# Kernel tuning notes

Hardware: AMD Instinct MI355X
Metric: run time of the kernel (lower is better)

## Reference

```python
import jax, jax.numpy as jnp
import numpy as np

K = 20
EPS = 1e-5
SLOPE = 0.2


def get_graph_feature(x, k):
    # x: [B, N, C]. DGCNN: knn on negative squared distance, gather, concat(nbr-ctr, ctr).
    sq = jnp.sum(x * x, axis=-1)                              # [B,N]
    inner = jnp.einsum('bnc,bmc->bnm', x, x)                  # [B,N,N]
    pdist = 2.0 * inner - sq[:, :, None] - sq[:, None, :]     # -||xi-xj||^2
    idx = jax.lax.top_k(pdist, k)[1]                          # [B,N,k] nearest (incl. self)
    b = jnp.arange(x.shape[0])[:, None, None]
    nbr = x[b, idx]                                           # [B,N,k,C]
    ctr = jnp.broadcast_to(x[:, :, None, :], nbr.shape)
    return jnp.concatenate([nbr - ctr, ctr], axis=-1)         # [B,N,k,2C]


def edgeconv(x, W, gamma, beta, mean, var):
    # 1x1 Conv2d (no bias) + BatchNorm2d (eval mode) + LeakyReLU(0.2) + max over k
    feat = get_graph_feature(x, K)                            # [B,N,k,2C]
    y = jnp.einsum('bnkc,oc->bnko', feat, W)                  # [B,N,k,O]
    y = (y - mean) * (gamma / jnp.sqrt(var + EPS)) + beta
    y = jnp.where(y >= 0, y, SLOPE * y)
    return jnp.max(y, axis=2)                                 # [B,N,O]


def dgcnn_pass(x, p1, p2, p3):
    x = edgeconv(x, *p1)
    x = edgeconv(x, *p2)
    x = edgeconv(x, *p3)
    return x                                                  # [B,N,F3]


def attention(emb, W_att):
    # SimGNN attention pooling (batched)
    ctx = jnp.tanh(jnp.mean(jnp.einsum('bnf,fg->bng', emb, W_att), axis=1))  # [B,F]
    s = jax.nn.sigmoid(jnp.einsum('bnf,bf->bn', emb, ctx))                   # [B,N]
    return jnp.einsum('bnf,bn->bf', emb, s)                                  # [B,F]


def tensor_network(e1, e2, W_t, W_block, bias):
    scoring = jnp.einsum('bf,fgt,bg->bt', e1, W_t, e2)        # [B,T]
    comb = jnp.concatenate([e1, e2], axis=1)                  # [B,2F]
    block = jnp.einsum('tf,bf->bt', W_block, comb)            # [B,T]
    return jax.nn.relu(scoring + block + bias)


def setup_inputs() -> dict:
    key = jax.random.key(0)
    ks = jax.random.split(key, 16)
    B, N, C = 8, 2048, 12
    F = 64
    T = 16
    d = {}
    d['graph1'] = jax.random.normal(ks[0], (B, N, C), jnp.float32)
    d['graph2'] = jax.random.normal(ks[1], (B, N, C), jnp.float32)
    d['W1'] = jax.random.normal(ks[2], (F, 2 * C), jnp.float32) * 0.1
    d['g1'] = jax.random.uniform(ks[3], (F,), jnp.float32, 0.5, 1.5)
    d['b1'] = jax.random.normal(ks[4], (F,), jnp.float32) * 0.1
    d['m1'] = jnp.zeros((F,), jnp.float32)
    d['v1'] = jnp.ones((F,), jnp.float32)
    d['W2'] = jax.random.normal(ks[5], (F, 2 * F), jnp.float32) * 0.1
    d['g2'] = jax.random.uniform(ks[6], (F,), jnp.float32, 0.5, 1.5)
    d['b2'] = jax.random.normal(ks[7], (F,), jnp.float32) * 0.1
    d['m2'] = jnp.zeros((F,), jnp.float32)
    d['v2'] = jnp.ones((F,), jnp.float32)
    d['W3'] = jax.random.normal(ks[8], (F, 2 * F), jnp.float32) * 0.1
    d['g3'] = jax.random.uniform(ks[9], (F,), jnp.float32, 0.5, 1.5)
    d['b3'] = jax.random.normal(ks[10], (F,), jnp.float32) * 0.1
    d['m3'] = jnp.zeros((F,), jnp.float32)
    d['v3'] = jnp.ones((F,), jnp.float32)
    d['W_att'] = jax.random.normal(ks[11], (F, F), jnp.float32) * 0.1
    d['W_tensor'] = jax.random.normal(ks[12], (F, F, T), jnp.float32) * 0.05
    d['W_block'] = jax.random.normal(ks[13], (T, 2 * F), jnp.float32) * 0.1
    d['bias_tn'] = jax.random.normal(ks[14], (T,), jnp.float32) * 0.1
    return d


def reference(graph1, graph2, W1, g1, b1, m1, v1, W2, g2, b2, m2, v2,
              W3, g3, b3, m3, v3, W_att, W_tensor, W_block, bias_tn):
    p1 = (W1, g1, b1, m1, v1)
    p2 = (W2, g2, b2, m2, v2)
    p3 = (W3, g3, b3, m3, v3)
    emb1 = dgcnn_pass(graph1, p1, p2, p3)   # [B,N,F]
    emb2 = dgcnn_pass(graph2, p1, p2, p3)
    e1 = attention(emb1, W_att)             # [B,F]
    e2 = attention(emb2, W_att)
    return tensor_network(e1, e2, W_tensor, W_block, bias_tn)  # [B,T]
```

## Files before the change

kernel.cpp:

```cpp
#include <hip/hip_runtime.h>
#include <hip/hip_bf16.h>
#include <float.h>

#define DEV __device__ __forceinline__

using f32x4 = __attribute__((ext_vector_type(4))) float;
using f4v   = __attribute__((ext_vector_type(4))) float;
using bfrag = __attribute__((ext_vector_type(8))) short;
using hfrag = __attribute__((ext_vector_type(8))) _Float16;
using us8   = __attribute__((ext_vector_type(8))) unsigned short;

DEV unsigned short f2bf(float f) {
  unsigned u = __builtin_bit_cast(unsigned, f);
  u += 0x7FFFu + ((u >> 16) & 1u);
  return (unsigned short)(u >> 16);
}
DEV float bf2f(unsigned short h) {
  unsigned u = ((unsigned)h) << 16;
  return __builtin_bit_cast(float, u);
}
DEV f32x4 mfma_bf(bfrag a, bfrag b, f32x4 c) {
  return __builtin_amdgcn_mfma_f32_16x16x32_bf16(a, b, c, 0, 0, 0);
}
DEV f32x4 mfma_h(hfrag a, hfrag b, f32x4 c) {
  return __builtin_amdgcn_mfma_f32_16x16x32_f16(a, b, c, 0, 0, 0);
}
DEV float readlane_f(float v, int l) {
  return __builtin_bit_cast(float,
      __builtin_amdgcn_readlane(__builtin_bit_cast(int, v), l));
}

template<int RB>
DEV unsigned swz(int row, int colb) {
  return (unsigned)(row * RB) +
         (((unsigned)colb) ^ (((unsigned)(row << 4)) & (unsigned)(RB - 1)));
}
template<int RB>
DEV bfrag ldfragB(const unsigned short* base, int row, int kcol) {
  return *(const bfrag*)((const char*)base + swz<RB>(row, kcol * 2));
}
template<int RB>
DEV hfrag ldfragH(const _Float16* base, int row, int kcol) {
  return *(const hfrag*)((const char*)base + swz<RB>(row, kcol * 2));
}

template<int BYTES>
DEV void cpyN(const char* __restrict__ g, char* __restrict__ l, int tid) {
  if constexpr (BYTES >= 8192) {
#pragma unroll
    for (int o = 0; o < BYTES; o += 8192)
      *(us8*)(l + o + tid * 16) = *(const us8*)(g + o + tid * 16);
  } else {
    const int o = tid * 16;
    if (o < BYTES) *(us8*)(l + o) = *(const us8*)(g + o);
  }
}

DEV void bitonic64(float& v, int& ix, int lane) {
#pragma unroll
  for (int k = 2; k <= 64; k <<= 1) {
#pragma unroll
    for (int j = k >> 1; j > 0; j >>= 1) {
      const float ov = __shfl_xor(v, j);
      const int   oi = __shfl_xor(ix, j);
      const bool up = (lane & k) != 0;
      const bool iWin = (v > ov) || (v == ov && ix < oi);
      const bool keepBetter = (((lane & j) == 0) != up);
      if (iWin != keepBetter) { v = ov; ix = oi; }
    }
  }
}

template<int C>
DEV const float* xbase(const float* xA, const float* xB, int b) {
  return (b < 8) ? xA + (size_t)b * 2048 * C
                 : xB + (size_t)(b - 8) * 2048 * C;
}

template<int C>
__global__ __launch_bounds__(256)
void sq_kernel(const float* __restrict__ xA, const float* __restrict__ xB,
               float* __restrict__ sq) {
  const int i = blockIdx.x * 256 + threadIdx.x;
  const int b = i >> 11, n = i & 2047;
  const float* r = xbase<C>(xA, xB, b) + (size_t)n * C;
  float s = 0.f;
#pragma unroll
  for (int c = 0; c < C; c += 4) {
    f4v v = *(const f4v*)(r + c);
    s += v[0] * v[0] + v[1] * v[1] + v[2] * v[2] + v[3] * v[3];
  }
  sq[i] = s;
}

template<int C, int C32>
__global__ __launch_bounds__(256)
void cvt_kernel(const float* __restrict__ xA, const float* __restrict__ xB,
                char* __restrict__ xhl) {
  constexpr int CH8 = C32 / 8, RB = C32 * 2, HB = 64 * RB;
  const int idx = blockIdx.x * 256 + threadIdx.x;
  const int chunk = idx & (CH8 - 1);
  const int rg = idx / CH8;
  const int b = rg >> 11, n = rg & 2047;
  const float* src = xbase<C>(xA, xB, b) + (size_t)n * C;
  const int cb = chunk * 8;
  float f[8];
  if constexpr (C % 8 == 0) {
    *(f4v*)(f + 0) = *(const f4v*)(src + cb);
    *(f4v*)(f + 4) = *(const f4v*)(src + cb + 4);
  } else {
#pragma unroll
    for (int e = 0; e < 8; ++e) {
      const int c = cb + e;
      f[e] = (c < C) ? src[c] : 0.f;
    }
  }
  us8 hv, lv;
#pragma unroll
  for (int e = 0; e < 8; ++e) {
    const unsigned short hs = f2bf(f[e]);
    hv[e] = hs;
    lv[e] = f2bf(f[e] - bf2f(hs));
  }
  char* dst = xhl + (size_t)(b * 32 + (n >> 6)) * 2 * HB;
  const unsigned off = swz<RB>(n & 63, cb * 2);
  *(us8*)(dst + off) = hv;
  *(us8*)(dst + HB + off) = lv;
}

template<int C32>
__global__ __launch_bounds__(512)
void knn_kernel(const char* __restrict__ xhl, const float* __restrict__ sqg,
                int* __restrict__ idx_out) {
  constexpr int N = 2048, TI = 32, TJ = 64, TK = 20, NT = N / TJ;
  constexpr int RB = C32 * 2, HB = 64 * RB, TILEB = 2 * HB, HBi = TI * RB;
  const int b    = blockIdx.x >> 6;
  const int it   = blockIdx.x & 63;
  const int i0   = it * TI;
  const int tid  = threadIdx.x;
  const int lane = tid & 63;
  const int w    = tid >> 6;
  const int ri   = w >> 2;
  const int ci   = w & 3;

  __shared__ us8 XiV[2 * HBi / 16];
  __shared__ us8 XjV[TILEB / 16];
  __shared__ float S[TI][TJ + 4];
  __shared__ float sqT[TJ];

  char* XiC = (char*)XiV;
  char* XjC = (char*)XjV;
  const unsigned short* XiHp = (const unsigned short*)XiC;
  const unsigned short* XiLp = (const unsigned short*)(XiC + HBi);
  const unsigned short* XjHp = (const unsigned short*)XjC;
  const unsigned short* XjLp = (const unsigned short*)(XjC + HB);
  const int m15 = lane & 15, kb8 = (lane >> 4) * 8;

  const char* gti = xhl + (size_t)(b * 32 + (i0 >> 6)) * TILEB + (i0 & 63) * RB;
  cpyN<HBi>(gti, XiC, tid);
  cpyN<HBi>(gti + HB, XiC + HBi, tid);

  float tv[4], t20[4]; int tix[4];
#pragma unroll
  for (int d = 0; d < 4; ++d) { tv[d] = -FLT_MAX; tix[d] = 0; t20[d] = -FLT_MAX; }

  for (int jt = 0; jt < NT; ++jt) {
    const char* gtj = xhl + (size_t)(b * 32 + jt) * TILEB;
    cpyN<TILEB>(gtj, XjC, tid);
    if (tid < TJ) sqT[tid] = sqg[b * N + jt * TJ + tid];
    __syncthreads();

    f32x4 acc = {0, 0, 0, 0};
#pragma unroll
    for (int ks = 0; ks < C32 / 32; ++ks) {
      const int kc = ks * 32 + kb8;
      const bfrag ah = ldfragB<RB>(XiHp, 16 * ri + m15, kc);
      const bfrag al = ldfragB<RB>(XiLp, 16 * ri + m15, kc);
      const bfrag bh = ldfragB<RB>(XjHp, 16 * ci + m15, kc);
      const bfrag bl = ldfragB<RB>(XjLp, 16 * ci + m15, kc);
      acc = mfma_bf(ah, bh, acc);
      acc = mfma_bf(ah, bl, acc);
      acc = mfma_bf(al, bh, acc);
    }
#pragma unroll
    for (int r = 0; r < 4; ++r)
      S[16 * ri + (lane >> 4) * 4 + r][16 * ci + m15] = acc[r];
    const float sqv = sqT[lane];
    __syncthreads();

    const int j0 = jt * TJ;
#pragma unroll
    for (int d = 0; d < 4; ++d) {
      const float sc = 2.f * S[4 * w + d][lane] - sqv;
      if (jt == 0) {
        float v = sc; int ixv = lane;
        bitonic64(v, ixv, lane);
        tv[d]  = (lane < TK) ? v : -FLT_MAX;
        tix[d] = (lane < TK) ? ixv : 0;
        t20[d] = readlane_f(tv[d], TK - 1);
      } else {
        unsigned long long mm = __ballot(sc > t20[d]);
        if (mm) {
          while (mm) {
            const int src = __ffsll(mm) - 1;
            mm &= mm - 1;
            const float cv = readlane_f(sc, src);
            const int   ci2 = j0 + src;
            const float pv_ = __shfl_up(tv[d], 1);
            const int   pi_ = __shfl_up(tix[d], 1);
            const unsigned long long g =
                __ballot(tv[d] > cv || (tv[d] == cv && tix[d] < ci2));
            const int p = __popcll(g);
            float nv = (lane == p) ? cv  : ((lane > p) ? pv_ : tv[d]);
            int   ni = (lane == p) ? ci2 : ((lane > p) ? pi_ : tix[d]);
            tv[d]  = (lane >= TK) ? -FLT_MAX : nv;
            tix[d] = (lane >= TK) ? 0 : ni;
          }
          t20[d] = readlane_f(tv[d], TK - 1);
        }
      }
    }
  }
  if (lane < TK) {
#pragma unroll
    for (int d = 0; d < 4; ++d) {
      const int i = i0 + 4 * w + d;
      idx_out[((size_t)b * N + i) * TK + lane] = tix[d];
    }
  }
}

template<int C, int C32>
__global__ __launch_bounds__(256)
void conv_kernel(const float* __restrict__ xA, const float* __restrict__ xB,
                 const int* __restrict__ idxg,
                 const float* __restrict__ W, const float* __restrict__ gam,
                 const float* __restrict__ bet, const float* __restrict__ mea,
                 const float* __restrict__ var, float* __restrict__ y) {
  constexpr int N = 2048, TK = 20, O = 64;
  constexpr int RB = C32 * 2;
  constexpr int CH8 = C32 / 8;
  const int b    = blockIdx.x >> 7;
  const int n0   = (blockIdx.x & 127) * 16;
  const int tid  = threadIdx.x;
  const int lane = tid & 63;
  const int w    = tid >> 6;

  __shared__ float    ctrF[16][C];
  __shared__ _Float16 A1[320 * C32];
  __shared__ _Float16 CtrB[16 * C32];
  __shared__ _Float16 WdT[O * C32];
  __shared__ _Float16 WcT[O * C32];

  const float* xb = xbase<C>(xA, xB, b);

  for (int i = tid; i < 16 * C; i += 256)
    ctrF[i / C][i % C] = xb[(size_t)(n0 + i / C) * C + (i % C)];

  for (int i = tid; i < O * CH8; i += 256) {
    const int o = i / CH8, ch = (i % CH8) * 8;
    hfrag hd, hc;
#pragma unroll
    for (int e = 0; e < 8; ++e) {
      const int c = ch + e;
      hd[e] = (c < C) ? (_Float16)W[o * 2 * C + c]     : (_Float16)0.f;
      hc[e] = (c < C) ? (_Float16)W[o * 2 * C + C + c] : (_Float16)0.f;
    }
    const unsigned off = swz<RB>(o, ch * 2);
    *(hfrag*)((char*)WdT + off) = hd;
    *(hfrag*)((char*)WcT + off) = hc;
  }
  __syncthreads();

  for (int i = tid; i < 16 * CH8; i += 256) {
    const int row = i / CH8, ch = (i % CH8) * 8;
    hfrag hv;
#pragma unroll
    for (int e = 0; e < 8; ++e) {
      const int c = ch + e;
      hv[e] = (c < C) ? (_Float16)ctrF[row][c] : (_Float16)0.f;
    }
    *(hfrag*)((char*)CtrB + swz<RB>(row, ch * 2)) = hv;
  }

  for (int r = tid; r < 16 * TK; r += 256) {
    const int n = r & 15, k = r >> 4;
    int j = idxg[((size_t)b * N + n0 + n) * TK + k];
    j &= (N - 1);
    const float* xj = xb + (size_t)j * C;
#pragma unroll
    for (int ch = 0; ch < C32; ch += 8) {
      float f[8];
#pragma unroll
      for (int q = 0; q < 8; q += 4) {
        const int c = ch + q;
        if (c + 3 < C) {
          *(f4v*)(f + q) = *(const f4v*)(xj + c);
        } else {
#pragma unroll
          for (int e = 0; e < 4; ++e) f[q + e] = (c + e < C) ? xj[c + e] : 0.f;
        }
      }
      hfrag hv;
#pragma unroll
      for (int e = 0; e < 8; ++e) {
        const int c = ch + e;
        const float d = (c < C) ? (f[e] - ctrF[n][c]) : 0.f;
        hv[e] = (_Float16)d;
      }
      *(hfrag*)((char*)A1 + swz<RB>(r, ch * 2)) = hv;
    }
  }
  __syncthreads();

  const int m15 = lane & 15;
  const int kb8 = (lane >> 4) * 8;
  hfrag bd[C32 / 32], bc[C32 / 32];
#pragma unroll
  for (int ks = 0; ks < C32 / 32; ++ks) {
    bd[ks] = ldfragH<RB>(WdT, 16 * w + m15, ks * 32 + kb8);
    bc[ks] = ldfragH<RB>(WcT, 16 * w + m15, ks * 32 + kb8);
  }
  f32x4 base = {0, 0, 0, 0};
#pragma unroll
  for (int ks = 0; ks < C32 / 32; ++ks)
    base = mfma_h(ldfragH<RB>(CtrB, m15, ks * 32 + kb8), bc[ks], base);

  f32x4 mx = {-FLT_MAX, -FLT_MAX, -FLT_MAX, -FLT_MAX};
#pragma unroll
  for (int k = 0; k < TK; ++k) {
    f32x4 a = {0, 0, 0, 0};
#pragma unroll
    for (int ks = 0; ks < C32 / 32; ++ks)
      a = mfma_h(ldfragH<RB>(A1, 16 * k + m15, ks * 32 + kb8), bd[ks], a);
#pragma unroll
    for (int r = 0; r < 4; ++r) mx[r] = fmaxf(mx[r], a[r] + base[r]);
  }

  const int o = 16 * w + m15;
  const float scv = gam[o] / sqrtf(var[o] + 1e-5f);
  const float shv = bet[o] - mea[o] * scv;
#pragma unroll
  for (int r = 0; r < 4; ++r) {
    const int n = (lane >> 4) * 4 + r;
    float v = scv * mx[r] + shv;
    v = (v >= 0.f) ? v : 0.2f * v;
    y[((size_t)b * N + n0 + n) * O + o] = v;
  }
}

__global__ __launch_bounds__(256)
void att_mean_kernel(const float* __restrict__ emb, float* __restrict__ msum) {
  constexpr int N = 2048, F = 64;
  const int b    = blockIdx.x >> 4;
  const int slab = blockIdx.x & 15;
  const int tid  = threadIdx.x;
  const int f = tid & 63, p = tid >> 6;
  __shared__ float part[4][F];
  float acc = 0.f;
  const float* e = emb + ((size_t)b * N + slab * 128) * F;
  for (int n = p; n < 128; n += 4) acc += e[(size_t)n * F + f];
  part[p][f] = acc;
  __syncthreads();
  if (tid < F)
    atomicAdd(&msum[b * F + tid],
              part[0][tid] + part[1][tid] + part[2][tid] + part[3][tid]);
}

__global__ __launch_bounds__(64)
void att_ctx_kernel(const float* __restrict__ msum, const float* __restrict__ Watt,
                    float* __restrict__ ctx) {
  constexpr int N = 2048, F = 64;
  const int b = blockIdx.x, tid = threadIdx.x;
  __shared__ float m[F];
  m[tid] = msum[b * F + tid] * (1.f / N);
  __syncthreads();
  float a = 0.f;
  for (int ff = 0; ff < F; ++ff) a += m[ff] * Watt[ff * F + tid];
  ctx[b * F + tid] = tanhf(a);
}

__global__ __launch_bounds__(256)
void att2_kernel(const float* __restrict__ emb, const float* __restrict__ ctx,
                 float* __restrict__ eout) {
  constexpr int N = 2048, F = 64;
  const int b   = blockIdx.x >> 3;
  const int c0  = (blockIdx.x & 7) * 256;
  const int tid = threadIdx.x, lane = tid & 63, w = tid >> 6;
  const float cv = ctx[b * F + lane];
  float acc = 0.f;
  const float* e = emb + (size_t)b * N * F;
  for (int n = c0 + w * 64; n < c0 + (w + 1) * 64; ++n) {
    const float v = e[(size_t)n * F + lane];
    float d = v * cv;
#pragma unroll
    for (int off = 1; off < 64; off <<= 1) d += __shfl_xor(d, off);
    const float s = 1.f / (1.f + expf(-d));
    acc += v * s;
  }
  atomicAdd(&eout[b * F + lane], acc);
}

__global__ __launch_bounds__(256)
void tn_kernel(const float* __restrict__ ep,
               const float* __restrict__ Wt, const float* __restrict__ Wb,
               const float* __restrict__ bias, float* __restrict__ out) {
  constexpr int F = 64, T = 16;
  const int b = blockIdx.x, tid = threadIdx.x;
  __shared__ float s1[F], s2[F];
  __shared__ float part[T][17];
  if (tid < F) { s1[tid] = ep[b * F + tid]; s2[tid] = ep[(b + 8) * F + tid]; }
  __syncthreads();
  const int t = tid >> 4, sub = tid & 15;
  float a = 0.f;
  for (int f = sub * 4; f < sub * 4 + 4; ++f) {
    float inner = 0.f;
    for (int g = 0; g < F; ++g) inner += Wt[((f * F) + g) * T + t] * s2[g];
    a += s1[f] * inner;
  }
  part[t][sub] = a;
  __syncthreads();
  if (tid < T) {
    float v = 0.f;
    for (int q = 0; q < 16; ++q) v += part[tid][q];
    for (int f = 0; f < F; ++f)
      v += Wb[tid * 2 * F + f] * s1[f] + Wb[tid * 2 * F + F + f] * s2[f];
    v += bias[tid];
    out[b * T + tid] = fmaxf(v, 0.f);
  }
}

extern "C" void kernel_launch(void* const* d_in, const int* in_sizes, int n_in,
                              void* d_out, int out_size, void* d_ws, size_t ws_size,
                              hipStream_t stream) {
  const float* x1  = (const float*)d_in[0];
  const float* x2  = (const float*)d_in[1];
  const float* W1  = (const float*)d_in[2];
  const float* g1  = (const float*)d_in[3];
  const float* b1  = (const float*)d_in[4];
  const float* m1  = (const float*)d_in[5];
  const float* v1  = (const float*)d_in[6];
  const float* W2  = (const float*)d_in[7];
  const float* g2  = (const float*)d_in[8];
  const float* b2  = (const float*)d_in[9];
  const float* m2  = (const float*)d_in[10];
  const float* v2  = (const float*)d_in[11];
  const float* W3  = (const float*)d_in[12];
  const float* g3  = (const float*)d_in[13];
  const float* b3  = (const float*)d_in[14];
  const float* m3  = (const float*)d_in[15];
  const float* v3  = (const float*)d_in[16];
  const float* Wat = (const float*)d_in[17];
  const float* Wt  = (const float*)d_in[18];
  const float* Wb  = (const float*)d_in[19];
  const float* bs  = (const float*)d_in[20];
  float* out = (float*)d_out;

  constexpr size_t NF = (size_t)16 * 2048 * 64;
  constexpr size_t XHLB = (size_t)16 * 32 * 16384;
  float* bufA = (float*)d_ws;
  float* bufB = bufA + NF;
  float* sqb  = bufB + NF;
  int*   idxb = (int*)(sqb + 16 * 2048);
  char*  xhl  = (char*)(idxb + (size_t)16 * 2048 * 20);
  float* msum = (float*)(xhl + XHLB);
  float* epool= msum + 16 * 64;
  float* ctx  = epool + 16 * 64;

  const float* bA8 = bufA + (size_t)8 * 2048 * 64;
  const float* bB8 = bufB + (size_t)8 * 2048 * 64;

  sq_kernel<12><<<128, 256, 0, stream>>>(x1, x2, sqb);
  cvt_kernel<12, 32><<<512, 256, 0, stream>>>(x1, x2, xhl);
  knn_kernel<32><<<1024, 512, 0, stream>>>(xhl, sqb, idxb);
  conv_kernel<12, 32><<<2048, 256, 0, stream>>>(x1, x2, idxb, W1, g1, b1, m1, v1, bufA);

  sq_kernel<64><<<128, 256, 0, stream>>>(bufA, bA8, sqb);
  cvt_kernel<64, 64><<<1024, 256, 0, stream>>>(bufA, bA8, xhl);
  knn_kernel<64><<<1024, 512, 0, stream>>>(xhl, sqb, idxb);
  conv_kernel<64, 64><<<2048, 256, 0, stream>>>(bufA, bA8, idxb, W2, g2, b2, m2, v2, bufB);

  sq_kernel<64><<<128, 256, 0, stream>>>(bufB, bB8, sqb);
  cvt_kernel<64, 64><<<1024, 256, 0, stream>>>(bufB, bB8, xhl);
  knn_kernel<64><<<1024, 512, 0, stream>>>(xhl, sqb, idxb);
  conv_kernel<64, 64><<<2048, 256, 0, stream>>>(bufB, bB8, idxb, W3, g3, b3, m3, v3, bufA);

  hipMemsetAsync(msum, 0, 2 * 16 * 64 * sizeof(float), stream);
  att_mean_kernel<<<256, 256, 0, stream>>>(bufA, msum);
  att_ctx_kernel<<<16, 64, 0, stream>>>(msum, Wat, ctx);
  att2_kernel<<<128, 256, 0, stream>>>(bufA, ctx, epool);
  tn_kernel<<<8, 256, 0, stream>>>(epool, Wt, Wb, bs, out);
}
```

Before: 937.4 us.

## Double-buffer KNN tiles with async global-to-LDS loads and deferred selection

Result: no change. 947.5 us (+1.1%).

```diff
diff --git a/kernel.cpp b/kernel.cpp
--- a/kernel.cpp
+++ b/kernel.cpp
@@ -29,6 +29,21 @@
   return __builtin_bit_cast(float,
       __builtin_amdgcn_readlane(__builtin_bit_cast(int, v), l));
 }
+DEV void glds16(const void* g, void* l) {
+  __builtin_amdgcn_global_load_lds(
+      (const __attribute__((address_space(1))) void*)g,
+      (__attribute__((address_space(3))) void*)l, 16, 0, 0);
+}
+template<int BYTES>
+DEV void gldsN(const char* __restrict__ g, char* __restrict__ l, int tid) {
+  if constexpr (BYTES >= 8192) {
+#pragma unroll
+    for (int o = 0; o < BYTES; o += 8192)
+      glds16(g + o + tid * 16, l + o + tid * 16);
+  } else {
+    if (tid * 16 < BYTES) glds16(g + tid * 16, l + tid * 16);
+  }
+}
 
 template<int RB>
 DEV unsigned swz(int row, int colb) {
@@ -42,18 +57,6 @@
 template<int RB>
 DEV hfrag ldfragH(const _Float16* base, int row, int kcol) {
   return *(const hfrag*)((const char*)base + swz<RB>(row, kcol * 2));
-}
-
-template<int BYTES>
-DEV void cpyN(const char* __restrict__ g, char* __restrict__ l, int tid) {
-  if constexpr (BYTES >= 8192) {
-#pragma unroll
-    for (int o = 0; o < BYTES; o += 8192)
-      *(us8*)(l + o + tid * 16) = *(const us8*)(g + o + tid * 16);
-  } else {
-    const int o = tid * 16;
-    if (o < BYTES) *(us8*)(l + o) = *(const us8*)(g + o);
-  }
 }
 
 DEV void bitonic64(float& v, int& ix, int lane) {
@@ -143,56 +146,41 @@
   const int ri   = w >> 2;
   const int ci   = w & 3;
 
-  __shared__ us8 XiV[2 * HBi / 16];
-  __shared__ us8 XjV[TILEB / 16];
-  __shared__ float S[TI][TJ + 4];
-  __shared__ float sqT[TJ];
-
-  char* XiC = (char*)XiV;
-  char* XjC = (char*)XjV;
+  __shared__ char XiC[2 * HBi];
+  __shared__ char XjC[2][TILEB];
+  __shared__ float S[2][TI][TJ + 4];
+
   const unsigned short* XiHp = (const unsigned short*)XiC;
   const unsigned short* XiLp = (const unsigned short*)(XiC + HBi);
-  const unsigned short* XjHp = (const unsigned short*)XjC;
-  const unsigned short* XjLp = (const unsigned short*)(XjC + HB);
   const int m15 = lane & 15, kb8 = (lane >> 4) * 8;
 
-  const char* gti = xhl + (size_t)(b * 32 + (i0 >> 6)) * TILEB + (i0 & 63) * RB;
-  cpyN<HBi>(gti, XiC, tid);
-  cpyN<HBi>(gti + HB, XiC + HBi, tid);
+  const char* gbt = xhl + (size_t)(b * 32) * TILEB;
+  const char* gti = gbt + (size_t)(i0 >> 6) * TILEB + (i0 & 63) * RB;
+  gldsN<HBi>(gti, XiC, tid);
+  gldsN<HBi>(gti + HB, XiC + HBi, tid);
+  gldsN<TILEB>(gbt, XjC[0], tid);
+  float sq_cur = sqg[b * N + lane];
+  float sq_prev = 0.f;
+  __syncthreads();
+
+  bfrag ah[C32 / 32], al[C32 / 32];
+#pragma unroll
+  for (int ks = 0; ks < C32 / 32; ++ks) {
+    ah[ks] = ldfragB<RB>(XiHp, 16 * ri + m15, ks * 32 + kb8);
+    al[ks] = ldfragB<RB>(XiLp, 16 * ri + m15, ks * 32 + kb8);
+  }
 
   float tv[4], t20[4]; int tix[4];
 #pragma unroll
   for (int d = 0; d < 4; ++d) { tv[d] = -FLT_MAX; tix[d] = 0; t20[d] = -FLT_MAX; }
 
-  for (int jt = 0; jt < NT; ++jt) {
-    const char* gtj = xhl + (size_t)(b * 32 + jt) * TILEB;
-    cpyN<TILEB>(gtj, XjC, tid);
-    if (tid < TJ) sqT[tid] = sqg[b * N + jt * TJ + tid];
-    __syncthreads();
-
-    f32x4 acc = {0, 0, 0, 0};
-#pragma unroll
-    for (int ks = 0; ks < C32 / 32; ++ks) {
-      const int kc = ks * 32 + kb8;
-      const bfrag ah = ldfragB<RB>(XiHp, 16 * ri + m15, kc);
-      const bfrag al = ldfragB<RB>(XiLp, 16 * ri + m15, kc);
-      const bfrag bh = ldfragB<RB>(XjHp, 16 * ci + m15, kc);
-      const bfrag bl = ldfragB<RB>(XjLp, 16 * ci + m15, kc);
-      acc = mfma_bf(ah, bh, acc);
-      acc = mfma_bf(ah, bl, acc);
-      acc = mfma_bf(al, bh, acc);
-    }
-#pragma unroll
-    for (int r = 0; r < 4; ++r)
-      S[16 * ri + (lane >> 4) * 4 + r][16 * ci + m15] = acc[r];
-    const float sqv = sqT[lane];
-    __syncthreads();
-
-    const int j0 = jt * TJ;
+  auto select_tile = [&](int jts, float sqv) {
+    const int j0 = jts * TJ;
+    const float (*Sb)[TJ + 4] = S[jts & 1];
 #pragma unroll
     for (int d = 0; d < 4; ++d) {
-      const float sc = 2.f * S[4 * w + d][lane] - sqv;
-      if (jt == 0) {
+      const float sc = 2.f * Sb[4 * w + d][lane] - sqv;
+      if (jts == 0) {
         float v = sc; int ixv = lane;
         bitonic64(v, ixv, lane);
         tv[d]  = (lane < TK) ? v : -FLT_MAX;
@@ -220,7 +208,37 @@
         }
       }
     }
-  }
+  };
+
+  for (int jt = 0; jt < NT; ++jt) {
+    float sq_next = 0.f;
+    if (jt + 1 < NT) {
+      gldsN<TILEB>(gbt + (size_t)(jt + 1) * TILEB, XjC[(jt + 1) & 1], tid);
+      sq_next = sqg[b * N + (jt + 1) * TJ + lane];
+    }
+    const unsigned short* XjHp = (const unsigned short*)XjC[jt & 1];
+    const unsigned short* XjLp = (const unsigned short*)(XjC[jt & 1] + HB);
+    f32x4 acc = {0, 0, 0, 0};
+#pragma unroll
+    for (int ks = 0; ks < C32 / 32; ++ks) {
+      const int kc = ks * 32 + kb8;
+      const bfrag bh = ldfragB<RB>(XjHp, 16 * ci + m15, kc);
+      const bfrag bl = ldfragB<RB>(XjLp, 16 * ci + m15, kc);
+      acc = mfma_bf(ah[ks], bh, acc);
+      acc = mfma_bf(ah[ks], bl, acc);
+      acc = mfma_bf(al[ks], bh, acc);
+    }
+#pragma unroll
+    for (int r = 0; r < 4; ++r)
+      S[jt & 1][16 * ri + (lane >> 4) * 4 + r][16 * ci + m15] = acc[r];
+
+    if (jt > 0) select_tile(jt - 1, sq_prev);
+
+    sq_prev = sq_cur; sq_cur = sq_next;
+    __syncthreads();
+  }
+  select_tile(NT - 1, sq_prev);
+
   if (lane < TK) {
 #pragma unroll
     for (int d = 0; d < 4; ++d) {
```
